# Kernel tuning notes

Measured on AMD Instinct MI355X. Metric: run time of the kernel, lower is better.

## Reference

```python
import jax, jax.numpy as jnp
import numpy as np

D_MODEL = 1024
N_HEADS = 16
HEAD_DIM = D_MODEL // N_HEADS  # 64
LATENT = 256
B, S = 2, 2048


def setup_inputs() -> dict:
    key = jax.random.key(0)
    ks = jax.random.split(key, 13)
    sc = 0.02
    inp = {
        'x': jax.random.normal(ks[0], (B, S, D_MODEL), jnp.float32),
        'Wq': jax.random.normal(ks[1], (D_MODEL, D_MODEL), jnp.float32) * sc,
        'bq': jnp.zeros((D_MODEL,), jnp.float32),
        'Wkd': jax.random.normal(ks[2], (D_MODEL, LATENT), jnp.float32) * sc,
        'bkd': jnp.zeros((LATENT,), jnp.float32),
        'Wvd': jax.random.normal(ks[3], (D_MODEL, LATENT), jnp.float32) * sc,
        'bvd': jnp.zeros((LATENT,), jnp.float32),
        'Wku': jax.random.normal(ks[4], (LATENT, D_MODEL), jnp.float32) * sc,
        'bku': jnp.zeros((D_MODEL,), jnp.float32),
        'Wvu': jax.random.normal(ks[5], (LATENT, D_MODEL), jnp.float32) * sc,
        'bvu': jnp.zeros((D_MODEL,), jnp.float32),
        'Wo': jax.random.normal(ks[6], (D_MODEL, D_MODEL), jnp.float32) * sc,
        'bo': jnp.zeros((D_MODEL,), jnp.float32),
    }
    return inp


def reference(x, Wq, bq, Wkd, bkd, Wvd, bvd, Wku, bku, Wvu, bvu, Wo, bo):
    b, s, _ = x.shape
    # projections
    Q = x @ Wq + bq                      # [b, s, d_model]
    K_latent = x @ Wkd + bkd             # [b, s, latent]
    V_latent = x @ Wvd + bvd             # [b, s, latent]
    K = K_latent @ Wku + bku             # [b, s, d_model]
    V = V_latent @ Wvu + bvu             # [b, s, d_model]
    # split heads
    Qh = Q.reshape(b, s, N_HEADS, HEAD_DIM)
    Kh = K.reshape(b, s, N_HEADS, HEAD_DIM)
    Vh = V.reshape(b, s, N_HEADS, HEAD_DIM)
    scale = 1.0 / jnp.sqrt(jnp.asarray(HEAD_DIM, x.dtype))
    scores = jnp.einsum('bqhd,bkhd->bhqk', Qh, Kh) * scale  # [b,h,s,s]
    attn = jax.nn.softmax(scores, axis=-1)
    ctx = jnp.einsum('bhqk,bkhd->bqhd', attn, Vh).reshape(b, s, D_MODEL)
    out = ctx @ Wo + bo
    return out
```

## Files before the change

### kernel.cpp

```cpp
#include <hip/hip_runtime.h>
#include <hip/hip_bf16.h>
#include <cstddef>

#define B_SZ 2
#define SEQ  2048
#define DM   1024
#define NH   16
#define HD   64
#define LAT  256
#define MTOT (B_SZ*SEQ)
#define NQKV 1536
#define QSCALE 0.18033688011112042f

typedef short bf16x8 __attribute__((ext_vector_type(8)));
typedef float floatx4 __attribute__((ext_vector_type(4)));
typedef unsigned short u16;

#if __has_builtin(__builtin_amdgcn_exp2f)
#define EXP2(x) __builtin_amdgcn_exp2f(x)
#else
#define EXP2(x) exp2f(x)
#endif

__device__ __forceinline__ u16 f2bf(float f) {
  union { float f; unsigned u; } a; a.f = f;
  unsigned r = a.u + 0x7FFFu + ((a.u >> 16) & 1u);
  return (u16)(r >> 16);
}

__device__ __forceinline__ floatx4 mfma16(bf16x8 a, bf16x8 b, floatx4 c) {
  return __builtin_amdgcn_mfma_f32_16x16x32_bf16(a, b, c, 0, 0, 0);
}

__device__ __forceinline__ void load16(const u16* g, u16* l) {
  __builtin_amdgcn_global_load_lds((const __attribute__((address_space(1))) unsigned*)g,
                                   (__attribute__((address_space(3))) unsigned*)l, 16, 0, 0);
}

__device__ void transpose_tile(const float* __restrict__ W, u16* __restrict__ WT,
                               int K, int N, int k0, int n0, u16 (*t)[65]) {
  const int r = threadIdx.x >> 4;
  const int c4 = (threadIdx.x & 15) * 4;
#pragma unroll
  for (int s = 0; s < 4; s++) {
    int row = s * 16 + r;
    float4 v = *(const float4*)&W[(size_t)(k0 + row) * N + n0 + c4];
    t[row][c4 + 0] = f2bf(v.x); t[row][c4 + 1] = f2bf(v.y);
    t[row][c4 + 2] = f2bf(v.z); t[row][c4 + 3] = f2bf(v.w);
  }
  __syncthreads();
  const int r2 = threadIdx.x >> 2;
  const int c8 = (threadIdx.x & 3) * 16;
  __align__(16) u16 tmp[16];
#pragma unroll
  for (int i = 0; i < 16; i++) tmp[i] = t[c8 + i][r2];
  u16* dst = WT + (size_t)(n0 + r2) * K + k0 + c8;
  *(bf16x8*)dst       = *(const bf16x8*)&tmp[0];
  *(bf16x8*)(dst + 8) = *(const bf16x8*)&tmp[8];
}

__global__ __launch_bounds__(256)
void prep_k(const float* __restrict__ x, u16* __restrict__ xb,
            const float* __restrict__ Wq, const float* __restrict__ Wkd,
            const float* __restrict__ Wvd, const float* __restrict__ Wku,
            const float* __restrict__ Wvu, const float* __restrict__ Wo,
            u16* __restrict__ WstkT, u16* __restrict__ WkuT,
            u16* __restrict__ WvuT, u16* __restrict__ WoT,
            const float* __restrict__ bq, const float* __restrict__ bkd,
            const float* __restrict__ bvd, float* __restrict__ bqkv) {
  __shared__ u16 t[64][65];
  const int blk = blockIdx.x;
  if (blk < 4096) {
    int i = blk * 256 + threadIdx.x;
    float4 v = ((const float4*)x)[i];
    ushort4 o; o.x = f2bf(v.x); o.y = f2bf(v.y); o.z = f2bf(v.z); o.w = f2bf(v.w);
    ((ushort4*)xb)[i] = o;
  } else if (blk < 4352) {
    int tt = blk - 4096;
    transpose_tile(Wq, WstkT, DM, DM, (tt >> 4) * 64, (tt & 15) * 64, t);
  } else if (blk < 4416) {
    int tt = blk - 4352;
    transpose_tile(Wkd, WstkT + (size_t)DM * DM, DM, LAT, (tt >> 2) * 64, (tt & 3) * 64, t);
  } else if (blk < 4480) {
    int tt = blk - 4416;
    transpose_tile(Wvd, WstkT + (size_t)1280 * DM, DM, LAT, (tt >> 2) * 64, (tt & 3) * 64, t);
  } else if (blk < 4544) {
    int tt = blk - 4480;
    transpose_tile(Wku, WkuT, LAT, DM, (tt >> 4) * 64, (tt & 15) * 64, t);
  } else if (blk < 4608) {
    int tt = blk - 4544;
    transpose_tile(Wvu, WvuT, LAT, DM, (tt >> 4) * 64, (tt & 15) * 64, t);
  } else if (blk < 4864) {
    int tt = blk - 4608;
    transpose_tile(Wo, WoT, DM, DM, (tt >> 4) * 64, (tt & 15) * 64, t);
  } else {
    int i = (blk - 4864) * 256 + threadIdx.x;
    float v = (i < 1024) ? bq[i] : (i < 1280) ? bkd[i - 1024] : bvd[i - 1280];
    bqkv[i] = v;
  }
}

template<int OUT_BF16, int VT1>
__global__ __launch_bounds__(256)
void gemm_bt(const u16* __restrict__ A0, const u16* __restrict__ A1,
             const u16* __restrict__ BT0, const u16* __restrict__ BT1,
             const float* __restrict__ bias0, const float* __restrict__ bias1,
             void* __restrict__ C0, void* __restrict__ C1,
             int M, int N, int Kd, int lda, float qscale, int qcols) {
  __shared__ u16 As[128 * 64];
  __shared__ u16 Bs[128 * 64];
  const u16* A  = blockIdx.z ? A1 : A0;
  const u16* BT = blockIdx.z ? BT1 : BT0;
  const float* bias = blockIdx.z ? bias1 : bias0;
  void* C = blockIdx.z ? C1 : C0;

  const int tid = threadIdx.x;
  const int m0 = blockIdx.y * 128, n0 = blockIdx.x * 128;
  const int wave = tid >> 6, lane = tid & 63;
  const int l15 = lane & 15, quad = lane >> 4;
  const int wm = (wave >> 1) * 64, wn = (wave & 1) * 64;

  floatx4 acc[4][4];
#pragma unroll
  for (int i = 0; i < 4; i++)
#pragma unroll
    for (int j = 0; j < 4; j++) acc[i][j] = (floatx4){0.f, 0.f, 0.f, 0.f};

  const int tr = tid >> 3;
  const int tc8 = (tid & 7) * 8;
  const u16* Ag = A  + (size_t)(m0 + tr) * lda + tc8;
  const u16* Bg = BT + (size_t)(n0 + tr) * Kd + tc8;
  u16* AsW = &As[(size_t)tid * 8];
  u16* BsW = &Bs[(size_t)tid * 8];

  for (int k0 = 0; k0 < Kd; k0 += 64) {
    __syncthreads();
#pragma unroll
    for (int s = 0; s < 4; s++) {
      load16(Ag + (size_t)(s * 32) * lda + k0, AsW + s * 2048);
      load16(Bg + (size_t)(s * 32) * Kd  + k0, BsW + s * 2048);
    }
    __syncthreads();
#pragma unroll
    for (int kk = 0; kk < 2; kk++) {
      bf16x8 af[4], bfr[4];
#pragma unroll
      for (int i = 0; i < 4; i++) {
        af[i]  = *(const bf16x8*)&As[(wm + i * 16 + l15) * 64 + kk * 32 + quad * 8];
        bfr[i] = *(const bf16x8*)&Bs[(wn + i * 16 + l15) * 64 + kk * 32 + quad * 8];
      }
#pragma unroll
      for (int i = 0; i < 4; i++)
#pragma unroll
        for (int j = 0; j < 4; j++)
          acc[i][j] = mfma16(af[i], bfr[j], acc[i][j]);
    }
  }

  if (VT1 && blockIdx.z == 1) {
#pragma unroll
    for (int i = 0; i < 4; i++) {
      int row = m0 + wm + i * 16 + quad * 4;
      int bb = row >> 11, sb = row & 2047;
#pragma unroll
      for (int j = 0; j < 4; j++) {
        int col = n0 + wn + j * 16 + l15;
        float bv = bias[col];
        union { u16 u[4]; uint2 w2; } tv;
#pragma unroll
        for (int r = 0; r < 4; r++) tv.u[r] = f2bf(acc[i][j][r] + bv);
        *(uint2*)((u16*)C + ((size_t)(bb * 16 + (col >> 6)) * 64 + (col & 63)) * SEQ + sb) = tv.w2;
      }
    }
  } else {
#pragma unroll
    for (int i = 0; i < 4; i++) {
      int row = m0 + wm + i * 16 + quad * 4;
#pragma unroll
      for (int j = 0; j < 4; j++) {
        int col = n0 + wn + j * 16 + l15;
        float bv = bias[col];
        float sc = (col < qcols) ? qscale : 1.f;
#pragma unroll
        for (int r = 0; r < 4; r++) {
          float v = (acc[i][j][r] + bv) * sc;
          if (OUT_BF16) ((u16*)C)[(size_t)(row + r) * N + col] = f2bf(v);
          else          ((float*)C)[(size_t)(row + r) * N + col] = v;
        }
      }
    }
  }
}

__global__ __launch_bounds__(256, 2)
void attn_fused(const u16* __restrict__ Q, const u16* __restrict__ K,
                const u16* __restrict__ VT, u16* __restrict__ CTX) {
  __shared__ float Ocmb[64][68];
  __shared__ float Lw[4][64];
  __shared__ u16 Plds[4][16][40];
  const int bh = blockIdx.y, b = bh >> 4, h = bh & 15;
  const int wave = threadIdx.x >> 6, lane = threadIdx.x & 63;
  const int l15 = lane & 15, quad = lane >> 4;
  const int q0 = blockIdx.x * 64;

  bf16x8 qf[4][2];
  {
    const u16* Qp = Q + (size_t)(b * SEQ + q0 + l15) * NQKV + h * HD + quad * 8;
#pragma unroll
    for (int qi = 0; qi < 4; qi++)
#pragma unroll
      for (int h2 = 0; h2 < 2; h2++)
        qf[qi][h2] = *(const bf16x8*)(Qp + (size_t)qi * 16 * NQKV + h2 * 32);
  }
  const u16* Kp = K + (size_t)(b * SEQ) * DM + h * HD + quad * 8;
  const u16* Vp = VT + ((size_t)bh * HD + l15) * SEQ + quad * 8;

  floatx4 o[4][4];
#pragma unroll
  for (int dt = 0; dt < 4; dt++)
#pragma unroll
    for (int qi = 0; qi < 4; qi++) o[dt][qi] = (floatx4){0.f, 0.f, 0.f, 0.f};
  float ls[4] = {0.f, 0.f, 0.f, 0.f};

  const int kb0 = wave * 512;

  for (int it = 0; it < 16; ++it) {
    const int kb = kb0 + it * 32;
    bf16x8 kf[2][2];
#pragma unroll
    for (int ki = 0; ki < 2; ki++)
#pragma unroll
      for (int h2 = 0; h2 < 2; h2++)
        kf[ki][h2] = *(const bf16x8*)(Kp + (size_t)(kb + ki * 16 + l15) * DM + h2 * 32);
    bf16x8 vf[4];
#pragma unroll
    for (int dt = 0; dt < 4; dt++)
      vf[dt] = *(const bf16x8*)(Vp + (size_t)(dt * 16) * SEQ + kb);

#pragma unroll
    for (int qi = 0; qi < 4; qi++) {
      unsigned pk[2][2];
#pragma unroll
      for (int ki = 0; ki < 2; ki++) {
        floatx4 z = (floatx4){0.f, 0.f, 0.f, 0.f};
        z = mfma16(kf[ki][0], qf[qi][0], z);
        z = mfma16(kf[ki][1], qf[qi][1], z);
        float p0 = EXP2(z[0]), p1 = EXP2(z[1]), p2 = EXP2(z[2]), p3 = EXP2(z[3]);
        ls[qi] += (p0 + p1) + (p2 + p3);
        unsigned u0 = __float_as_uint(p0) + 0x8000u;
        unsigned u1 = __float_as_uint(p1) + 0x8000u;
        unsigned u2 = __float_as_uint(p2) + 0x8000u;
        unsigned u3 = __float_as_uint(p3) + 0x8000u;
        pk[ki][0] = __builtin_amdgcn_perm(u1, u0, 0x07060302u);
        pk[ki][1] = __builtin_amdgcn_perm(u3, u2, 0x07060302u);
      }
      {
        uint2 w0; w0.x = pk[0][0]; w0.y = pk[0][1];
        *(uint2*)&Plds[wave][l15][quad * 4] = w0;
        uint2 w1; w1.x = pk[1][0]; w1.y = pk[1][1];
        *(uint2*)&Plds[wave][l15][16 + quad * 4] = w1;
      }
      bf16x8 pf = *(const bf16x8*)&Plds[wave][l15][quad * 8];
#pragma unroll
      for (int dt = 0; dt < 4; dt++)
        o[dt][qi] = mfma16(vf[dt], pf, o[dt][qi]);
    }
  }

#pragma unroll
  for (int qi = 0; qi < 4; qi++) {
    float v = ls[qi];
    v += __shfl_xor(v, 16);
    v += __shfl_xor(v, 32);
    if (quad == 0) Lw[wave][qi * 16 + l15] = v;
  }
  if (wave == 0) {
#pragma unroll
    for (int dt = 0; dt < 4; dt++)
#pragma unroll
      for (int qi = 0; qi < 4; qi++)
        *(floatx4*)&Ocmb[qi * 16 + l15][dt * 16 + quad * 4] = o[dt][qi];
  }
  __syncthreads();
  if (wave == 1) {
#pragma unroll
    for (int dt = 0; dt < 4; dt++)
#pragma unroll
      for (int qi = 0; qi < 4; qi++) {
        floatx4* pp = (floatx4*)&Ocmb[qi * 16 + l15][dt * 16 + quad * 4];
        *pp = *pp + o[dt][qi];
      }
  }
  __syncthreads();
  if (wave == 2) {
#pragma unroll
    for (int dt = 0; dt < 4; dt++)
#pragma unroll
      for (int qi = 0; qi < 4; qi++) {
        floatx4* pp = (floatx4*)&Ocmb[qi * 16 + l15][dt * 16 + quad * 4];
        *pp = *pp + o[dt][qi];
      }
  }
  __syncthreads();
  if (wave == 3) {
#pragma unroll
    for (int qi = 0; qi < 4; qi++) {
      int qq = qi * 16 + l15;
      float lt = Lw[0][qq] + Lw[1][qq] + Lw[2][qq] + Lw[3][qq];
      float inv = 1.f / lt;
      u16* Crow = CTX + (size_t)(b * SEQ + q0 + qq) * DM + h * HD + quad * 4;
#pragma unroll
      for (int dt = 0; dt < 4; dt++) {
        floatx4 ov = o[dt][qi] + *(const floatx4*)&Ocmb[qq][dt * 16 + quad * 4];
        union { u16 u[4]; uint2 w2; } tv;
#pragma unroll
        for (int r = 0; r < 4; r++) tv.u[r] = f2bf(ov[r] * inv);
        *(uint2*)(Crow + dt * 16) = tv.w2;
      }
    }
  }
}

extern "C" void kernel_launch(void* const* d_in, const int* in_sizes, int n_in,
                              void* d_out, int out_size, void* d_ws, size_t ws_size,
                              hipStream_t stream) {
  const float* x   = (const float*)d_in[0];
  const float* Wq  = (const float*)d_in[1];
  const float* bq  = (const float*)d_in[2];
  const float* Wkd = (const float*)d_in[3];
  const float* bkd = (const float*)d_in[4];
  const float* Wvd = (const float*)d_in[5];
  const float* bvd = (const float*)d_in[6];
  const float* Wku = (const float*)d_in[7];
  const float* bku = (const float*)d_in[8];
  const float* Wvu = (const float*)d_in[9];
  const float* bvu = (const float*)d_in[10];
  const float* Wo  = (const float*)d_in[11];
  const float* bo  = (const float*)d_in[12];
  float* out = (float*)d_out;

  float* bqkv = (float*)d_ws;
  u16* p = (u16*)((char*)d_ws + 1536 * sizeof(float));
  u16* xb    = p; p += (size_t)MTOT * DM;
  u16* WstkT = p; p += (size_t)NQKV * DM;
  u16* WkuT  = p; p += (size_t)DM * LAT;
  u16* WvuT  = p; p += (size_t)DM * LAT;
  u16* WoT   = p; p += (size_t)DM * DM;
  u16* QKVb  = p; p += (size_t)MTOT * NQKV;
  u16* Kb    = p; p += (size_t)MTOT * DM;
  u16* VTb   = p; p += (size_t)MTOT * DM;
  u16* CXb   = p; p += (size_t)MTOT * DM;

  prep_k<<<4870, 256, 0, stream>>>(x, xb, Wq, Wkd, Wvd, Wku, Wvu, Wo,
                                   WstkT, WkuT, WvuT, WoT, bq, bkd, bvd, bqkv);

  gemm_bt<1, 0><<<dim3(NQKV / 128, MTOT / 128, 1), 256, 0, stream>>>(
      xb, xb, WstkT, WstkT, bqkv, bqkv, QKVb, QKVb, MTOT, NQKV, DM, DM, QSCALE, DM);
  gemm_bt<1, 1><<<dim3(DM / 128, MTOT / 128, 2), 256, 0, stream>>>(
      QKVb + 1024, QKVb + 1280, WkuT, WvuT, bku, bvu, Kb, VTb, MTOT, DM, LAT, NQKV, 1.f, 0);

  attn_fused<<<dim3(SEQ / 64, B_SZ * NH), 256, 0, stream>>>(QKVb, Kb, VTb, CXb);

  gemm_bt<0, 0><<<dim3(DM / 128, MTOT / 128, 1), 256, 0, stream>>>(
      CXb, CXb, WoT, WoT, bo, bo, out, out, MTOT, DM, DM, DM, 1.f, 0);
}
```

Measured before the change: 235.5 us.

## Shrink GEMM tiles for more blocks and double-buffer K/V loads in attention

The GEMM kernel is templated on the M tile, with N tiles cut to 64. QKV and up-projection GEMMs use 128x64 tiles and the output projection uses 64x64, which launches more blocks across the CUs. In attention, K/V fragments for the next 32-key chunk are prefetched into registers while the current chunk computes. P writes to LDS are also batched for all four query subtiles before the PV MFMAs. The cost is more register pressure in attention, a larger LDS buffer, and less data reuse per GEMM block.

```diff
diff --git a/kernel.cpp b/kernel.cpp
--- a/kernel.cpp
+++ b/kernel.cpp
@@ -100,31 +100,32 @@
   }
 }
 
-template<int OUT_BF16, int VT1>
+template<int TM, int OUT_BF16, int VT1>
 __global__ __launch_bounds__(256)
 void gemm_bt(const u16* __restrict__ A0, const u16* __restrict__ A1,
              const u16* __restrict__ BT0, const u16* __restrict__ BT1,
              const float* __restrict__ bias0, const float* __restrict__ bias1,
              void* __restrict__ C0, void* __restrict__ C1,
              int M, int N, int Kd, int lda, float qscale, int qcols) {
-  __shared__ u16 As[128 * 64];
-  __shared__ u16 Bs[128 * 64];
+  constexpr int FM = TM / 32;
+  __shared__ u16 As[TM * 64];
+  __shared__ u16 Bs[64 * 64];
   const u16* A  = blockIdx.z ? A1 : A0;
   const u16* BT = blockIdx.z ? BT1 : BT0;
   const float* bias = blockIdx.z ? bias1 : bias0;
   void* C = blockIdx.z ? C1 : C0;
 
   const int tid = threadIdx.x;
-  const int m0 = blockIdx.y * 128, n0 = blockIdx.x * 128;
+  const int m0 = blockIdx.y * TM, n0 = blockIdx.x * 64;
   const int wave = tid >> 6, lane = tid & 63;
   const int l15 = lane & 15, quad = lane >> 4;
-  const int wm = (wave >> 1) * 64, wn = (wave & 1) * 64;
-
-  floatx4 acc[4][4];
-#pragma unroll
-  for (int i = 0; i < 4; i++)
-#pragma unroll
-    for (int j = 0; j < 4; j++) acc[i][j] = (floatx4){0.f, 0.f, 0.f, 0.f};
+  const int wm = (wave >> 1) * (TM / 2), wn = (wave & 1) * 32;
+
+  floatx4 acc[FM][2];
+#pragma unroll
+  for (int i = 0; i < FM; i++)
+#pragma unroll
+    for (int j = 0; j < 2; j++) acc[i][j] = (floatx4){0.f, 0.f, 0.f, 0.f};
 
   const int tr = tid >> 3;
   const int tc8 = (tid & 7) * 8;
@@ -136,34 +137,36 @@
   for (int k0 = 0; k0 < Kd; k0 += 64) {
     __syncthreads();
 #pragma unroll
-    for (int s = 0; s < 4; s++) {
+    for (int s = 0; s < FM; s++)
       load16(Ag + (size_t)(s * 32) * lda + k0, AsW + s * 2048);
+#pragma unroll
+    for (int s = 0; s < 2; s++)
       load16(Bg + (size_t)(s * 32) * Kd  + k0, BsW + s * 2048);
-    }
     __syncthreads();
 #pragma unroll
     for (int kk = 0; kk < 2; kk++) {
-      bf16x8 af[4], bfr[4];
-#pragma unroll
-      for (int i = 0; i < 4; i++) {
+      bf16x8 af[FM], bfr[2];
+#pragma unroll
+      for (int i = 0; i < FM; i++)
         af[i]  = *(const bf16x8*)&As[(wm + i * 16 + l15) * 64 + kk * 32 + quad * 8];
-        bfr[i] = *(const bf16x8*)&Bs[(wn + i * 16 + l15) * 64 + kk * 32 + quad * 8];
-      }
-#pragma unroll
-      for (int i = 0; i < 4; i++)
-#pragma unroll
-        for (int j = 0; j < 4; j++)
+#pragma unroll
+      for (int j = 0; j < 2; j++)
+        bfr[j] = *(const bf16x8*)&Bs[(wn + j * 16 + l15) * 64 + kk * 32 + quad * 8];
+#pragma unroll
+      for (int i = 0; i < FM; i++)
+#pragma unroll
+        for (int j = 0; j < 2; j++)
           acc[i][j] = mfma16(af[i], bfr[j], acc[i][j]);
     }
   }
 
   if (VT1 && blockIdx.z == 1) {
 #pragma unroll
-    for (int i = 0; i < 4; i++) {
+    for (int i = 0; i < FM; i++) {
       int row = m0 + wm + i * 16 + quad * 4;
       int bb = row >> 11, sb = row & 2047;
 #pragma unroll
-      for (int j = 0; j < 4; j++) {
+      for (int j = 0; j < 2; j++) {
         int col = n0 + wn + j * 16 + l15;
         float bv = bias[col];
         union { u16 u[4]; uint2 w2; } tv;
@@ -174,10 +177,10 @@
     }
   } else {
 #pragma unroll
-    for (int i = 0; i < 4; i++) {
+    for (int i = 0; i < FM; i++) {
       int row = m0 + wm + i * 16 + quad * 4;
 #pragma unroll
-      for (int j = 0; j < 4; j++) {
+      for (int j = 0; j < 2; j++) {
         int col = n0 + wn + j * 16 + l15;
         float bv = bias[col];
         float sc = (col < qcols) ? qscale : 1.f;
@@ -197,7 +200,7 @@
                 const u16* __restrict__ VT, u16* __restrict__ CTX) {
   __shared__ float Ocmb[64][68];
   __shared__ float Lw[4][64];
-  __shared__ u16 Plds[4][16][40];
+  __shared__ u16 Plds[4][64][40];
   const int bh = blockIdx.y, b = bh >> 4, h = bh & 15;
   const int wave = threadIdx.x >> 6, lane = threadIdx.x & 63;
   const int l15 = lane & 15, quad = lane >> 4;
@@ -224,46 +227,62 @@
 
   const int kb0 = wave * 512;
 
+  bf16x8 kfb[2][2][2], vfb[2][4];
+#pragma unroll
+  for (int ki = 0; ki < 2; ki++)
+#pragma unroll
+    for (int h2 = 0; h2 < 2; h2++)
+      kfb[0][ki][h2] = *(const bf16x8*)(Kp + (size_t)(kb0 + ki * 16 + l15) * DM + h2 * 32);
+#pragma unroll
+  for (int dt = 0; dt < 4; dt++)
+    vfb[0][dt] = *(const bf16x8*)(Vp + (size_t)(dt * 16) * SEQ + kb0);
+
+#pragma unroll 2
   for (int it = 0; it < 16; ++it) {
+    const int cur = it & 1, nxt = cur ^ 1;
     const int kb = kb0 + it * 32;
-    bf16x8 kf[2][2];
-#pragma unroll
-    for (int ki = 0; ki < 2; ki++)
-#pragma unroll
-      for (int h2 = 0; h2 < 2; h2++)
-        kf[ki][h2] = *(const bf16x8*)(Kp + (size_t)(kb + ki * 16 + l15) * DM + h2 * 32);
-    bf16x8 vf[4];
-#pragma unroll
-    for (int dt = 0; dt < 4; dt++)
-      vf[dt] = *(const bf16x8*)(Vp + (size_t)(dt * 16) * SEQ + kb);
-
+    if (it < 15) {
+      const int kn = kb + 32;
+#pragma unroll
+      for (int ki = 0; ki < 2; ki++)
+#pragma unroll
+        for (int h2 = 0; h2 < 2; h2++)
+          kfb[nxt][ki][h2] = *(const bf16x8*)(Kp + (size_t)(kn + ki * 16 + l15) * DM + h2 * 32);
+#pragma unroll
+      for (int dt = 0; dt < 4; dt++)
+        vfb[nxt][dt] = *(const bf16x8*)(Vp + (size_t)(dt * 16) * SEQ + kn);
+    }
+    unsigned pw[4][4];
 #pragma unroll
     for (int qi = 0; qi < 4; qi++) {
-      unsigned pk[2][2];
 #pragma unroll
       for (int ki = 0; ki < 2; ki++) {
         floatx4 z = (floatx4){0.f, 0.f, 0.f, 0.f};
-        z = mfma16(kf[ki][0], qf[qi][0], z);
-        z = mfma16(kf[ki][1], qf[qi][1], z);
+        z = mfma16(kfb[cur][ki][0], qf[qi][0], z);
+        z = mfma16(kfb[cur][ki][1], qf[qi][1], z);
         float p0 = EXP2(z[0]), p1 = EXP2(z[1]), p2 = EXP2(z[2]), p3 = EXP2(z[3]);
         ls[qi] += (p0 + p1) + (p2 + p3);
         unsigned u0 = __float_as_uint(p0) + 0x8000u;
         unsigned u1 = __float_as_uint(p1) + 0x8000u;
         unsigned u2 = __float_as_uint(p2) + 0x8000u;
         unsigned u3 = __float_as_uint(p3) + 0x8000u;
-        pk[ki][0] = __builtin_amdgcn_perm(u1, u0, 0x07060302u);
-        pk[ki][1] = __builtin_amdgcn_perm(u3, u2, 0x07060302u);
-      }
-      {
-        uint2 w0; w0.x = pk[0][0]; w0.y = pk[0][1];
-        *(uint2*)&Plds[wave][l15][quad * 4] = w0;
-        uint2 w1; w1.x = pk[1][0]; w1.y = pk[1][1];
-        *(uint2*)&Plds[wave][l15][16 + quad * 4] = w1;
-      }
-      bf16x8 pf = *(const bf16x8*)&Plds[wave][l15][quad * 8];
+        pw[qi][ki * 2]     = __builtin_amdgcn_perm(u1, u0, 0x07060302u);
+        pw[qi][ki * 2 + 1] = __builtin_amdgcn_perm(u3, u2, 0x07060302u);
+      }
+    }
+#pragma unroll
+    for (int qi = 0; qi < 4; qi++) {
+      uint2 w0; w0.x = pw[qi][0]; w0.y = pw[qi][1];
+      *(uint2*)&Plds[wave][qi * 16 + l15][quad * 4] = w0;
+      uint2 w1; w1.x = pw[qi][2]; w1.y = pw[qi][3];
+      *(uint2*)&Plds[wave][qi * 16 + l15][16 + quad * 4] = w1;
+    }
+#pragma unroll
+    for (int qi = 0; qi < 4; qi++) {
+      bf16x8 pf = *(const bf16x8*)&Plds[wave][qi * 16 + l15][quad * 8];
 #pragma unroll
       for (int dt = 0; dt < 4; dt++)
-        o[dt][qi] = mfma16(vf[dt], pf, o[dt][qi]);
+        o[dt][qi] = mfma16(vfb[cur][dt], pf, o[dt][qi]);
     }
   }
 
@@ -354,13 +373,13 @@
   prep_k<<<4870, 256, 0, stream>>>(x, xb, Wq, Wkd, Wvd, Wku, Wvu, Wo,
                                    WstkT, WkuT, WvuT, WoT, bq, bkd, bvd, bqkv);
 
-  gemm_bt<1, 0><<<dim3(NQKV / 128, MTOT / 128, 1), 256, 0, stream>>>(
+  gemm_bt<128, 1, 0><<<dim3(NQKV / 64, MTOT / 128, 1), 256, 0, stream>>>(
       xb, xb, WstkT, WstkT, bqkv, bqkv, QKVb, QKVb, MTOT, NQKV, DM, DM, QSCALE, DM);
-  gemm_bt<1, 1><<<dim3(DM / 128, MTOT / 128, 2), 256, 0, stream>>>(
+  gemm_bt<128, 1, 1><<<dim3(DM / 64, MTOT / 128, 2), 256, 0, stream>>>(
       QKVb + 1024, QKVb + 1280, WkuT, WvuT, bku, bvu, Kb, VTb, MTOT, DM, LAT, NQKV, 1.f, 0);
 
   attn_fused<<<dim3(SEQ / 64, B_SZ * NH), 256, 0, stream>>>(QKVb, Kb, VTb, CXb);
 
-  gemm_bt<0, 0><<<dim3(DM / 128, MTOT / 128, 1), 256, 0, stream>>>(
+  gemm_bt<64, 0, 0><<<dim3(DM / 64, MTOT / 64, 1), 256, 0, stream>>>(
       CXb, CXb, WoT, WoT, bo, bo, out, out, MTOT, DM, DM, DM, 1.f, 0);
 }
```

Result: faster. 223.3 us (-5.2%).
